# Kernel optimization log

Measured on AMD Instinct MI355X. Metric: run time of the kernel, lower is better.

Reference implementation:

```python
import jax, jax.numpy as jnp
import numpy as np

NF = 64      # feature channels
DG = 8       # deformable groups
KH = 3       # kernel size
K = KH * KH  # kernel points
B, H, W = 2, 256, 256


def conv2d(x, w, b):
    # 3x3, stride 1, pad 1, NCHW
    y = jax.lax.conv_general_dilated(x, w, (1, 1), [(1, 1), (1, 1)],
                                     dimension_numbers=('NCHW', 'OIHW', 'NCHW'))
    return y + b[None, :, None, None]


def bilinear_gather(img, py, px):
    # img: [B,G,Cg,H,W]; py,px: [B,G,Kd,H,W] float pixel coords (zero padding outside)
    # returns [B,G,Cg,Kd,H,W]
    b, g, cg, h, w = img.shape
    kd = py.shape[2]
    y0 = jnp.floor(py)
    x0 = jnp.floor(px)
    wy = py - y0
    wx = px - x0
    imgf = img.reshape(b, g, cg, h * w)

    def tap(yi, xi, wt):
        valid = (yi >= 0) & (yi <= h - 1) & (xi >= 0) & (xi <= w - 1)
        idx = (jnp.clip(yi, 0, h - 1) * w + jnp.clip(xi, 0, w - 1)).astype(jnp.int32)
        idxf = idx.reshape(b, g, 1, kd * h * w)
        v = jnp.take_along_axis(imgf, jnp.broadcast_to(idxf, (b, g, cg, kd * h * w)), axis=-1)
        v = v.reshape(b, g, cg, kd, h, w)
        return v * (wt * valid)[:, :, None]

    return (tap(y0, x0, (1 - wy) * (1 - wx)) + tap(y0, x0 + 1, (1 - wy) * wx)
            + tap(y0 + 1, x0, wy * (1 - wx)) + tap(y0 + 1, x0 + 1, wy * wx))


def setup_inputs() -> dict:
    key = jax.random.key(0)
    ks = jax.random.split(key, 8)
    s = 0.05
    return {
        'nbr': jax.random.normal(ks[0], (B, NF, H, W), jnp.float32),
        'ref': jax.random.normal(ks[1], (B, NF, H, W), jnp.float32),
        'optical_flow': jax.random.normal(ks[2], (B, 2, H, W), jnp.float32),
        'conv1_w': jax.random.normal(ks[3], (NF, 2 * NF, KH, KH), jnp.float32) * s,
        'conv1_b': jnp.zeros((NF,), jnp.float32),
        'om_w': jax.random.normal(ks[4], (DG * 3 * K, NF + 2, KH, KH), jnp.float32) * s,
        'om_b': jnp.zeros((DG * 3 * K,), jnp.float32),
        'dcn_w': jax.random.normal(ks[5], (NF, NF, KH, KH), jnp.float32) * s,
        'dcn_b': jnp.zeros((NF,), jnp.float32),
    }


def reference(nbr, ref, optical_flow, conv1_w, conv1_b, om_w, om_b, dcn_w, dcn_b):
    b, c, h, w = nbr.shape
    dt = nbr.dtype
    gy, gx = jnp.meshgrid(jnp.arange(h, dtype=dt), jnp.arange(w, dtype=dt), indexing='ij')

    # ---- backwarp(nbr, flow): bilinear sample at (x+fx, y+fy), zero padding ----
    py = (gy[None] + optical_flow[:, 1])[:, None, None]  # [B,1,1,H,W]
    px = (gx[None] + optical_flow[:, 0])[:, None, None]
    nbr_warp = bilinear_gather(nbr[:, None], py, px).reshape(b, c, h, w)

    # ---- offset feature ----
    fea = jax.nn.relu(conv2d(jnp.concatenate([nbr_warp, ref], 1), conv1_w, conv1_b))

    # ---- FlowGuidedDCN offset/mask generation ----
    out = conv2d(jnp.concatenate([fea, optical_flow], 1), om_w, om_b)
    o1, o2, mask = jnp.split(out, 3, axis=1)
    offset = jnp.concatenate([o1, o2], 1)                       # [B, 2*DG*K, H, W]
    flow_rep = jnp.tile(optical_flow[:, ::-1], (1, offset.shape[1] // 2, 1, 1))
    offset = offset + flow_rep
    mask = jax.nn.sigmoid(mask)                                 # [B, DG*K, H, W]

    # ---- deformable conv v2 (stride 1, pad 1, dil 1) ----
    off = offset.reshape(b, DG, K, 2, h, w)
    dy, dx = off[:, :, :, 0], off[:, :, :, 1]                   # [B,DG,K,H,W]
    ky, kx = jnp.meshgrid(jnp.arange(KH, dtype=dt), jnp.arange(KH, dtype=dt), indexing='ij')
    base_y = gy[None] - 1 + ky.reshape(-1)[:, None, None]       # [K,H,W]
    base_x = gx[None] - 1 + kx.reshape(-1)[:, None, None]
    spy = base_y[None, None] + dy
    spx = base_x[None, None] + dx

    cg = c // DG
    sampled = bilinear_gather(nbr.reshape(b, DG, cg, h, w), spy, spx)  # [B,DG,Cg,K,H,W]
    m = mask.reshape(b, DG, 1, K, h, w)
    wr = dcn_w.reshape(dcn_w.shape[0], DG, cg, K)
    y = jnp.einsum('bgckhw,ogck->bohw', sampled * m, wr) + dcn_b[None, :, None, None]
    return y
```

## Files before the change

kernel.cpp:

```cpp
#include <hip/hip_runtime.h>
#include <math.h>

#define HW 65536
#define WD 256
#define HT 256

typedef short short8 __attribute__((ext_vector_type(8)));
typedef short sh4 __attribute__((ext_vector_type(4)));
typedef float f32x4 __attribute__((ext_vector_type(4)));
typedef __bf16 bf16x8 __attribute__((ext_vector_type(8)));
typedef __bf16 bf16x4 __attribute__((ext_vector_type(4)));

__device__ __forceinline__ short f2bf(float f) {
    union { float f; unsigned u; } v; v.f = f;
    unsigned r = (v.u + 0x7fffu + ((v.u >> 16) & 1u)) >> 16;
    return (short)r;
}

__device__ __forceinline__ float bf2f(short s) {
    union { unsigned u; float f; } v;
    v.u = ((unsigned)(unsigned short)s) << 16;
    return v.f;
}

__device__ __forceinline__ int iclamp(int v, int lo, int hi) {
    return v < lo ? lo : (v > hi ? hi : v);
}

struct Taps {
    int i00, i01, i10, i11;
    float w00, w01, w10, w11;
};

__device__ __forceinline__ Taps make_taps(float py, float px) {
    float fy0 = floorf(py), fx0 = floorf(px);
    float wy = py - fy0, wx = px - fx0;
    int y0 = (int)fy0, x0 = (int)fx0;
    int y1 = y0 + 1, x1 = x0 + 1;
    float vy0 = (y0 >= 0 && y0 <= HT - 1) ? 1.f : 0.f;
    float vy1 = (y1 >= 0 && y1 <= HT - 1) ? 1.f : 0.f;
    float vx0 = (x0 >= 0 && x0 <= WD - 1) ? 1.f : 0.f;
    float vx1 = (x1 >= 0 && x1 <= WD - 1) ? 1.f : 0.f;
    int yc0 = iclamp(y0, 0, HT - 1), yc1 = iclamp(y1, 0, HT - 1);
    int xc0 = iclamp(x0, 0, WD - 1), xc1 = iclamp(x1, 0, WD - 1);
    Taps t;
    t.i00 = yc0 * WD + xc0; t.i01 = yc0 * WD + xc1;
    t.i10 = yc1 * WD + xc0; t.i11 = yc1 * WD + xc1;
    t.w00 = (1.f - wy) * (1.f - wx) * vy0 * vx0;
    t.w01 = (1.f - wy) * wx * vy0 * vx1;
    t.w10 = wy * (1.f - wx) * vy1 * vx0;
    t.w11 = wy * wx * vy1 * vx1;
    return t;
}

__global__ __launch_bounds__(256) void pack_nbr_kernel(
    const float* __restrict__ nbr, short* __restrict__ N2)
{
    __shared__ short tile[64 * 66];
    int blk = blockIdx.x;
    int b = blk >> 10;
    int grp = blk & 1023;
    int px = threadIdx.x & 63;
    int qq = threadIdx.x >> 6;
    int pos = grp * 64 + px;

    const float* nb = nbr + (size_t)b * 64 * HW;
    #pragma unroll
    for (int j = 0; j < 16; ++j) {
        int c = qq * 16 + j;
        tile[px * 66 + c] = f2bf(nb[c * HW + pos]);
    }
    __syncthreads();

    short* xo = N2 + (size_t)b * HW * 64;
    #pragma unroll
    for (int f8 = threadIdx.x; f8 < 512; f8 += 256) {
        int g = f8 >> 6;
        int p = f8 & 63;
        short8 v;
        #pragma unroll
        for (int j = 0; j < 8; ++j) v[j] = tile[p * 66 + g * 8 + j];
        *(short8*)(xo + ((size_t)g * HW + grp * 64 + p) * 8) = v;
    }
}

__global__ __launch_bounds__(256) void pack_x1_kernel(
    const short* __restrict__ N2, const float* __restrict__ ref,
    const float* __restrict__ flow, short* __restrict__ X1)
{
    __shared__ short tile[64 * 136];
    int blk = blockIdx.x;
    int b = blk >> 10;
    int grp = blk & 1023;
    int px = threadIdx.x & 63;
    int qq = threadIdx.x >> 6;
    int pos = grp * 64 + px;
    int yy = pos >> 8, xx = pos & 255;

    float fx = flow[b * 2 * HW + pos];
    float fy = flow[b * 2 * HW + HW + pos];
    Taps tp = make_taps((float)yy + fy, (float)xx + fx);

    const short* n2b = N2 + (size_t)b * HW * 64;
    const float* rf = ref + (size_t)b * 64 * HW;

    #pragma unroll
    for (int gi = 0; gi < 2; ++gi) {
        int g = qq * 2 + gi;
        const short* nbg = n2b + (size_t)g * HW * 8;
        short8 a00 = *(const short8*)(nbg + (size_t)tp.i00 * 8);
        short8 a01 = *(const short8*)(nbg + (size_t)tp.i01 * 8);
        short8 a10 = *(const short8*)(nbg + (size_t)tp.i10 * 8);
        short8 a11 = *(const short8*)(nbg + (size_t)tp.i11 * 8);
        union { bf16x8 bv; short8 s; } u;
        #pragma unroll
        for (int c = 0; c < 8; ++c) {
            float s = tp.w00 * bf2f(a00[c]) + tp.w01 * bf2f(a01[c]) +
                      tp.w10 * bf2f(a10[c]) + tp.w11 * bf2f(a11[c]);
            u.bv[c] = (__bf16)s;
        }
        *(short8*)(&tile[px * 136 + g * 8]) = u.s;
    }
    #pragma unroll
    for (int j = 0; j < 16; ++j) {
        int c = qq * 16 + j;
        tile[px * 136 + 64 + c] = f2bf(rf[c * HW + pos]);
    }
    __syncthreads();

    short* xo = X1 + ((size_t)b * HW + grp * 64) * 128;
    #pragma unroll
    for (int f8 = threadIdx.x; f8 < 1024; f8 += 256) {
        int p = (f8 * 8) >> 7;
        int c = (f8 * 8) & 127;
        short8 v;
        #pragma unroll
        for (int j = 0; j < 8; ++j) v[j] = tile[p * 136 + c + j];
        *(short8*)(xo + f8 * 8) = v;
    }
}

__global__ __launch_bounds__(256) void repack_w1_kernel(
    const float* __restrict__ w, short* __restrict__ wr)
{
    int t = blockIdx.x * 256 + threadIdx.x;
    int j = t & 7, q = (t >> 3) & 3, l = (t >> 5) & 15;
    int nt = (t >> 9) & 3, kc = t >> 11;
    int k = kc * 32 + q * 8 + j;
    int rs = k >> 7, c = k & 127;
    int n = nt * 16 + l;
    wr[t] = f2bf(w[(n * 128 + c) * 9 + rs]);
}

__global__ __launch_bounds__(256) void repack_w2_kernel(
    const float* __restrict__ w, short* __restrict__ wr)
{
    int t = blockIdx.x * 256 + threadIdx.x;
    if (t >= 155648) return;
    int j = t & 7, q = (t >> 3) & 3, l = (t >> 5) & 15;
    int nt = (t >> 9) & 15, kc = t >> 13;
    int n = nt * 16 + l;
    float v = 0.f;
    if (kc < 18) {
        int k = kc * 32 + q * 8 + j;
        int rs = k >> 6, c = k & 63;
        if (n < 216) v = w[(n * 66 + c) * 9 + rs];
    } else {
        int k18 = q * 8 + j;
        if (k18 < 18 && n < 216) {
            int tap = k18 >> 1, u = k18 & 1;
            v = w[(n * 66 + 64 + u) * 9 + tap];
        }
    }
    wr[t] = f2bf(v);
}

__global__ __launch_bounds__(256) void repack_dcn_kernel(
    const float* __restrict__ w, short* __restrict__ wr)
{
    int t = blockIdx.x * 256 + threadIdx.x;
    int j = t & 7, q = (t >> 3) & 3, l = (t >> 5) & 15;
    int rem = t >> 9;
    int nt = rem & 3;
    int gkc = rem >> 2;
    int kc = gkc % 3, g = gkc / 3;
    int Kidx = kc * 32 + q * 8 + j;
    int k = Kidx >> 3, c = Kidx & 7;
    int och = nt * 16 + l;
    float v = (k < 9) ? w[(och * 64 + g * 8 + c) * 9 + k] : 0.f;
    wr[t] = f2bf(v);
}

#define PADC1 128
__global__ __launch_bounds__(256) void conv1_mfma_kernel(
    const short* __restrict__ X1, const float* __restrict__ bias,
    const short* __restrict__ wr, short* __restrict__ X2)
{
    __shared__ short lds[198 * PADC1];
    const int tid = threadIdx.x;
    const int w = __builtin_amdgcn_readfirstlane(tid >> 6);
    const int l15 = tid & 15;
    const int q = (tid >> 4) & 3;
    const int blk = ((blockIdx.x & 7) << 8) | (blockIdx.x >> 3);
    const int xseg = blk & 3;
    const int yy = (blk >> 2) & 255;
    const int b = blk >> 10;
    const int x0 = xseg * 64;

    const short* xin = X1 + (size_t)b * HW * 128;
    for (int i = tid; i < 198 * 16; i += 256) {
        int c16 = i & 15;
        int pix = i >> 4;
        int r = pix / 66, xx = pix % 66;
        int gy = yy + r - 1, gx = x0 + xx - 1;
        short8 v = {0, 0, 0, 0, 0, 0, 0, 0};
        if (gy >= 0 && gy < HT && gx >= 0 && gx < WD)
            v = *(const short8*)(xin + ((size_t)((gy << 8) + gx)) * 128 + c16 * 8);
        *(short8*)(&lds[pix * PADC1 + (c16 ^ (pix & 7)) * 8]) = v;
    }
    __syncthreads();

    f32x4 acc[4] = {{0,0,0,0},{0,0,0,0},{0,0,0,0},{0,0,0,0}};
    const int bbase = l15 * 4 + q;

    #define LOADB1(kc_) (*(const short8*)(wr + ((size_t)(((kc_) * 4 + w) * 64 + bbase)) * 8))
    #define COMP1(kc_, bf_) { \
        int rs_ = (kc_) >> 2, cc_ = (kc_) & 3; \
        int r_ = rs_ / 3, s_ = rs_ % 3; \
        int rowb_ = r_ * 66 + s_ + l15; \
        _Pragma("unroll") \
        for (int mt = 0; mt < 4; ++mt) { \
            int row_ = rowb_ + mt * 16; \
            int col16_ = (cc_ * 4 + q) ^ (row_ & 7); \
            short8 a_ = *(const short8*)(&lds[row_ * PADC1 + col16_ * 8]); \
            acc[mt] = __builtin_amdgcn_mfma_f32_16x16x32_bf16(a_, bf_, acc[mt], 0, 0, 0); \
        } }

    short8 bA = LOADB1(0), bB;
    #pragma unroll 1
    for (int jj = 0; jj < 18; ++jj) {
        int kc0 = 2 * jj;
        bB = LOADB1(kc0 + 1);
        COMP1(kc0, bA);
        int kc2 = kc0 + 2; if (kc2 > 35) kc2 = 35;
        bA = LOADB1(kc2);
        COMP1(kc0 + 1, bB);
    }
    #undef LOADB1
    #undef COMP1

    float bv = bias[w * 16 + l15];
    short* xo = X2 + (size_t)b * HW * 64;
    #pragma unroll
    for (int mt = 0; mt < 4; ++mt) {
        #pragma unroll
        for (int rg = 0; rg < 4; ++rg) {
            int px = x0 + mt * 16 + q * 4 + rg;
            float v = fmaxf(acc[mt][rg] + bv, 0.f);
            xo[((size_t)((yy << 8) + px)) * 64 + w * 16 + l15] = f2bf(v);
        }
    }
}

#define PADX2 64
__global__ __launch_bounds__(256, 2) void om_mfma_kernel(
    const short* __restrict__ X2, const float* __restrict__ flow,
    const short* __restrict__ wr, const float* __restrict__ bias,
    float* __restrict__ OFF, short* __restrict__ MB)
{
    __shared__ __align__(16) char ldsraw[67584];
    short* ldsA = (short*)ldsraw;
    short* A18  = (short*)(ldsraw + 49920);
    float* ldsT = (float*)ldsraw;

    const int tid = threadIdx.x;
    const int w = __builtin_amdgcn_readfirstlane(tid >> 6);
    const int l15 = tid & 15;
    const int q = (tid >> 4) & 3;
    const int blk = ((blockIdx.x & 7) << 7) | (blockIdx.x >> 3);
    const int xseg = blk & 1;
    const int yy = (blk >> 1) & 255;
    const int b = blk >> 9;
    const int x0 = xseg * 128;

    const short* xin = X2 + (size_t)b * HW * 64;
    #pragma unroll
    for (int r = 0; r < 3; ++r) {
        int gy = yy + r - 1;
        for (int i = tid; i < 130 * 8; i += 256) {
            int xx = i >> 3, c8 = i & 7;
            int gx = x0 + xx - 1;
            short8 v = {0, 0, 0, 0, 0, 0, 0, 0};
            if (gy >= 0 && gy < HT && gx >= 0 && gx < WD)
                v = *(const short8*)(xin + ((size_t)((gy << 8) + gx)) * 64 + c8 * 8);
            int pix = r * 130 + xx;
            *(short8*)(&ldsA[pix * PADX2 + (c8 ^ (pix & 7)) * 8]) = v;
        }
    }
    for (int i = tid; i < 128 * 32; i += 256) {
        int p = i >> 5, kk = i & 31;
        short v = 0;
        if (kk < 18) {
            int tap = kk >> 1, u = kk & 1;
            int gy = yy + tap / 3 - 1, gx = x0 + p + tap % 3 - 1;
            if (gy >= 0 && gy < HT && gx >= 0 && gx < WD)
                v = f2bf(flow[(size_t)(b * 2 + u) * HW + (gy << 8) + gx]);
        }
        A18[p * 34 + kk] = v;
    }
    __syncthreads();

    f32x4 acc[4][8];
    #pragma unroll
    for (int i = 0; i < 4; ++i)
        #pragma unroll
        for (int mt = 0; mt < 8; ++mt) acc[i][mt] = (f32x4){0, 0, 0, 0};

    const int bbase = l15 * 4 + q;

    #define LOADB2(dst_, kc_) { \
        _Pragma("unroll") \
        for (int i = 0; i < 4; ++i) \
            dst_[i] = *(const short8*)(wr + ((size_t)(((kc_) * 16 + w * 4 + i) * 64 + bbase)) * 8); }
    #define COMP2(kc_, bf_) { \
        int rs_ = (kc_) >> 1, half_ = (kc_) & 1; \
        int r_ = rs_ / 3, s_ = rs_ % 3; \
        int rowb_ = r_ * 130 + s_ + l15; \
        _Pragma("unroll") \
        for (int mt = 0; mt < 8; ++mt) { \
            int row_ = rowb_ + mt * 16; \
            int col16_ = (half_ * 4 + q) ^ (row_ & 7); \
            short8 a_ = *(const short8*)(&ldsA[row_ * PADX2 + col16_ * 8]); \
            _Pragma("unroll") \
            for (int i = 0; i < 4; ++i) \
                acc[i][mt] = __builtin_amdgcn_mfma_f32_16x16x32_bf16(a_, bf_[i], acc[i][mt], 0, 0, 0); \
        } }

    short8 bA[4], bB[4];
    LOADB2(bA, 0);
    #pragma unroll 1
    for (int jj = 0; jj < 9; ++jj) {
        int kc0 = 2 * jj;
        LOADB2(bB, kc0 + 1);
        COMP2(kc0, bA);
        LOADB2(bA, kc0 + 2);
        COMP2(kc0 + 1, bB);
    }
    #pragma unroll
    for (int mt = 0; mt < 8; ++mt) {
        short8 a_ = *(const short8*)(&A18[(mt * 16 + l15) * 34 + q * 8]);
        #pragma unroll
        for (int i = 0; i < 4; ++i)
            acc[i][mt] = __builtin_amdgcn_mfma_f32_16x16x32_bf16(a_, bA[i], acc[i][mt], 0, 0, 0);
    }
    #undef LOADB2
    #undef COMP2

    #pragma unroll 1
    for (int pass = 0; pass < 2; ++pass) {
        __syncthreads();
        if ((w >> 1) == pass) {
            int ochl_base = (w & 1) * 64;
            #pragma unroll
            for (int i = 0; i < 4; ++i) {
                int ochl = ochl_base + i * 16 + l15;
                #pragma unroll
                for (int mt = 0; mt < 8; ++mt)
                    #pragma unroll
                    for (int rg = 0; rg < 4; ++rg)
                        ldsT[ochl * 132 + mt * 16 + q * 4 + rg] = acc[i][mt][rg];
            }
        }
        __syncthreads();
        for (int f = tid; f < 128 * 32; f += 256) {
            int chl = f >> 5, p16 = (f & 31) * 4;
            int ch = pass * 128 + chl;
            if (ch < 216) {
                f32x4 v = *(const f32x4*)(&ldsT[chl * 132 + p16]);
                float bv = bias[ch];
                if (ch < 144) {
                    v[0] += bv; v[1] += bv; v[2] += bv; v[3] += bv;
                    *(f32x4*)(&OFF[((size_t)b * 144 + ch) * HW + (yy << 8) + x0 + p16]) = v;
                } else {
                    union { bf16x4 bv4; sh4 s4; } u;
                    #pragma unroll
                    for (int j = 0; j < 4; ++j) {
                        float m = 1.f / (1.f + __expf(-(v[j] + bv)));
                        u.bv4[j] = (__bf16)m;
                    }
                    *(sh4*)(&MB[((size_t)b * 72 + (ch - 144)) * HW + (yy << 8) + x0 + p16]) = u.s4;
                }
            }
        }
    }
}

__global__ __launch_bounds__(256) void dcn_mfma_kernel(
    const float* __restrict__ OFF,
    const short* __restrict__ MB,
    const float* __restrict__ flow,
    const short* __restrict__ N2,
    const short* __restrict__ wrd,
    const float* __restrict__ bias,
    float* __restrict__ out)
{
    __shared__ __align__(16) char ldsraw[26624];
    short* bufA = (short*)ldsraw;
    short* bufB = (short*)(ldsraw + 13312);
    float* ldsT = (float*)ldsraw;

    const int tid = threadIdx.x;
    const int w = __builtin_amdgcn_readfirstlane(tid >> 6);
    const int l15 = tid & 15;
    const int q = (tid >> 4) & 3;
    const int qq = tid >> 6;
    const int px = tid & 63;

    const int blk = ((blockIdx.x & 7) << 8) | (blockIdx.x >> 3);
    const int b = blk >> 10;
    const int grp = blk & 1023;
    const int pos0 = grp * 64;
    const int pos = pos0 + px;
    const int yy = pos >> 8, xx = pos & 255;

    const float* offb = OFF + (size_t)b * 144 * HW + pos;
    const short* mbp  = MB + (size_t)b * 72 * HW + pos;
    const float fx = flow[b * 2 * HW + pos];
    const float fy = flow[b * 2 * HW + HW + pos];
    const short* n2b = N2 + (size_t)b * HW * 64;

    {
        short8 z = {0, 0, 0, 0, 0, 0, 0, 0};
        #pragma unroll
        for (int it = 0; it < 3; ++it) {
            int k = qq + 4 * it;
            if (k >= 9) {
                *(short8*)(&bufA[px * 104 + k * 8]) = z;
                *(short8*)(&bufB[px * 104 + k * 8]) = z;
            }
        }
    }

    f32x4 acc[4] = {{0,0,0,0},{0,0,0,0},{0,0,0,0},{0,0,0,0}};

    float rdy[3], rdx[3];
    short rms[3];
    #pragma unroll
    for (int it = 0; it < 3; ++it) {
        int k = qq + 4 * it;
        rdy[it] = 0.f; rdx[it] = 0.f; rms[it] = 0;
        if (k < 9) {
            rdy[it] = offb[(size_t)(2 * k) * HW];
            rdx[it] = offb[(size_t)(2 * k + 1) * HW];
            rms[it] = mbp[(size_t)k * HW];
        }
    }

    {
        const short* nbg = n2b;
        float w00[3], w01[3], w10[3], w11[3];
        short8 a00[3], a01[3], a10[3], a11[3];
        #pragma unroll
        for (int it = 0; it < 3; ++it) {
            int k = qq + 4 * it;
            if (k < 9) {
                float dy = rdy[it] + fy, dx = rdx[it] + fx;
                float m = bf2f(rms[it]);
                Taps tp = make_taps((float)(yy - 1 + k / 3) + dy,
                                    (float)(xx - 1 + k % 3) + dx);
                w00[it] = tp.w00 * m; w01[it] = tp.w01 * m;
                w10[it] = tp.w10 * m; w11[it] = tp.w11 * m;
                a00[it] = *(const short8*)(nbg + (size_t)tp.i00 * 8);
                a01[it] = *(const short8*)(nbg + (size_t)tp.i01 * 8);
                a10[it] = *(const short8*)(nbg + (size_t)tp.i10 * 8);
                a11[it] = *(const short8*)(nbg + (size_t)tp.i11 * 8);
            }
        }
        #pragma unroll
        for (int it = 0; it < 3; ++it) {
            int k = qq + 4 * it;
            if (k < 9) {
                rdy[it] = offb[(size_t)(18 + 2 * k) * HW];
                rdx[it] = offb[(size_t)(18 + 2 * k + 1) * HW];
                rms[it] = mbp[(size_t)(9 + k) * HW];
            }
        }
        #pragma unroll
        for (int it = 0; it < 3; ++it) {
            int k = qq + 4 * it;
            if (k < 9) {
                union { bf16x8 bv; short8 s; } u;
                #pragma unroll
                for (int c = 0; c < 8; ++c) {
                    float s = w00[it] * bf2f(a00[it][c]) + w01[it] * bf2f(a01[it][c]) +
                              w10[it] * bf2f(a10[it][c]) + w11[it] * bf2f(a11[it][c]);
                    u.bv[c] = (__bf16)s;
                }
                *(short8*)(&bufA[px * 104 + k * 8]) = u.s;
            }
        }
    }
    __syncthreads();

    #pragma unroll 1
    for (int g = 0; g < 8; ++g) {
        short* cur = (g & 1) ? bufB : bufA;
        short* nxt = (g & 1) ? bufA : bufB;

        float w00[3], w01[3], w10[3], w11[3];
        short8 a00[3], a01[3], a10[3], a11[3];
        if (g < 7) {
            const short* nbg = n2b + (size_t)(g + 1) * HW * 8;
            #pragma unroll
            for (int it = 0; it < 3; ++it) {
                int k = qq + 4 * it;
                if (k < 9) {
                    float dy = rdy[it] + fy, dx = rdx[it] + fx;
                    float m = bf2f(rms[it]);
                    Taps tp = make_taps((float)(yy - 1 + k / 3) + dy,
                                        (float)(xx - 1 + k % 3) + dx);
                    w00[it] = tp.w00 * m; w01[it] = tp.w01 * m;
                    w10[it] = tp.w10 * m; w11[it] = tp.w11 * m;
                    a00[it] = *(const short8*)(nbg + (size_t)tp.i00 * 8);
                    a01[it] = *(const short8*)(nbg + (size_t)tp.i01 * 8);
                    a10[it] = *(const short8*)(nbg + (size_t)tp.i10 * 8);
                    a11[it] = *(const short8*)(nbg + (size_t)tp.i11 * 8);
                }
            }
            if (g < 6) {
                #pragma unroll
                for (int it = 0; it < 3; ++it) {
                    int k = qq + 4 * it;
                    if (k < 9) {
                        rdy[it] = offb[(size_t)((g + 2) * 18 + 2 * k) * HW];
                        rdx[it] = offb[(size_t)((g + 2) * 18 + 2 * k + 1) * HW];
                        rms[it] = mbp[(size_t)((g + 2) * 9 + k) * HW];
                    }
                }
            }
        }

        #pragma unroll
        for (int kc = 0; kc < 3; ++kc) {
            short8 bfrag = *(const short8*)(wrd +
                ((size_t)(((g * 3 + kc) * 4 + w) * 64 + l15 * 4 + q)) * 8);
            #pragma unroll
            for (int mt = 0; mt < 4; ++mt) {
                short8 a = *(const short8*)(&cur[(mt * 16 + l15) * 104 + kc * 32 + q * 8]);
                acc[mt] = __builtin_amdgcn_mfma_f32_16x16x32_bf16(a, bfrag, acc[mt], 0, 0, 0);
            }
        }

        if (g < 7) {
            #pragma unroll
            for (int it = 0; it < 3; ++it) {
                int k = qq + 4 * it;
                if (k < 9) {
                    union { bf16x8 bv; short8 s; } u;
                    #pragma unroll
                    for (int c = 0; c < 8; ++c) {
                        float s = w00[it] * bf2f(a00[it][c]) + w01[it] * bf2f(a01[it][c]) +
                                  w10[it] * bf2f(a10[it][c]) + w11[it] * bf2f(a11[it][c]);
                        u.bv[c] = (__bf16)s;
                    }
                    *(short8*)(&nxt[px * 104 + k * 8]) = u.s;
                }
            }
        }
        __syncthreads();
    }

    #pragma unroll
    for (int mt = 0; mt < 4; ++mt)
        *(f32x4*)(&ldsT[(w * 16 + l15) * 68 + mt * 16 + q * 4]) = acc[mt];
    __syncthreads();
    float* ob = out + (size_t)b * 64 * HW + pos0;
    #pragma unroll
    for (int f = tid; f < 1024; f += 256) {
        int och = f >> 4, p4 = (f & 15) * 4;
        f32x4 v = *(const f32x4*)(&ldsT[och * 68 + p4]);
        float bv = bias[och];
        v[0] += bv; v[1] += bv; v[2] += bv; v[3] += bv;
        *(f32x4*)(&ob[(size_t)och * HW + p4]) = v;
    }
}

extern "C" void kernel_launch(void* const* d_in, const int* in_sizes, int n_in,
                              void* d_out, int out_size, void* d_ws, size_t ws_size,
                              hipStream_t stream)
{
    const float* nbr  = (const float*)d_in[0];
    const float* ref  = (const float*)d_in[1];
    const float* flow = (const float*)d_in[2];
    const float* c1w  = (const float*)d_in[3];
    const float* c1b  = (const float*)d_in[4];
    const float* omw  = (const float*)d_in[5];
    const float* omb  = (const float*)d_in[6];
    const float* dw   = (const float*)d_in[7];
    const float* db   = (const float*)d_in[8];
    float* out = (float*)d_out;

    char* wsb = (char*)d_ws;
    short* X1    = (short*)(wsb);
    short* X2    = (short*)(wsb + 33554432);
    short* N2    = (short*)(wsb + 50331648);
    float* OFF   = (float*)(wsb + 67108864);
    short* MB    = (short*)(wsb + 142606336);
    short* wr1   = (short*)(wsb + 161480704);
    short* wr2   = (short*)(wsb + 161628160);
    short* wrd   = (short*)(wsb + 161939456);

    repack_w1_kernel<<<288, 256, 0, stream>>>(c1w, wr1);
    repack_w2_kernel<<<608, 256, 0, stream>>>(omw, wr2);
    repack_dcn_kernel<<<192, 256, 0, stream>>>(dw, wrd);
    pack_nbr_kernel<<<2048, 256, 0, stream>>>(nbr, N2);
    pack_x1_kernel<<<2048, 256, 0, stream>>>(N2, ref, flow, X1);
    conv1_mfma_kernel<<<2048, 256, 0, stream>>>(X1, c1b, wr1, X2);
    om_mfma_kernel<<<1024, 256, 0, stream>>>(X2, flow, wr2, omb, OFF, MB);
    dcn_mfma_kernel<<<2048, 256, 0, stream>>>(OFF, MB, flow, N2, wrd, db, out);
}
```

Measured before the change: 325.4 us.

## Retile conv1 so each block computes four rows with all output channels per wave

The conv1 MFMA kernel now has each block cover four output rows by 64 pixels instead of one row, with each wave owning one row and all 64 output channels. Input channels are staged through shared memory in two halves of 64. This cuts redundant halo loads across blocks (6 input rows for 4 outputs instead of 3 for 1) and reuses each A fragment across four B tiles. The grid shrinks from 2048 to 512 blocks, and the 64 accumulators per lane raise register pressure, which may reduce occupancy.

```diff
diff --git a/kernel.cpp b/kernel.cpp
--- a/kernel.cpp
+++ b/kernel.cpp
@@ -191,73 +191,93 @@
     wr[t] = f2bf(v);
 }
 
-#define PADC1 128
 __global__ __launch_bounds__(256) void conv1_mfma_kernel(
     const short* __restrict__ X1, const float* __restrict__ bias,
     const short* __restrict__ wr, short* __restrict__ X2)
 {
-    __shared__ short lds[198 * PADC1];
+    __shared__ short lds[396 * 64];
     const int tid = threadIdx.x;
     const int w = __builtin_amdgcn_readfirstlane(tid >> 6);
     const int l15 = tid & 15;
     const int q = (tid >> 4) & 3;
-    const int blk = ((blockIdx.x & 7) << 8) | (blockIdx.x >> 3);
+    const int blk = ((blockIdx.x & 7) << 6) | (blockIdx.x >> 3);
     const int xseg = blk & 3;
-    const int yy = (blk >> 2) & 255;
-    const int b = blk >> 10;
+    const int yq = (blk >> 2) & 63;
+    const int b = blk >> 8;
     const int x0 = xseg * 64;
+    const int y0r = yq * 4;
 
     const short* xin = X1 + (size_t)b * HW * 128;
-    for (int i = tid; i < 198 * 16; i += 256) {
-        int c16 = i & 15;
-        int pix = i >> 4;
-        int r = pix / 66, xx = pix % 66;
-        int gy = yy + r - 1, gx = x0 + xx - 1;
-        short8 v = {0, 0, 0, 0, 0, 0, 0, 0};
-        if (gy >= 0 && gy < HT && gx >= 0 && gx < WD)
-            v = *(const short8*)(xin + ((size_t)((gy << 8) + gx)) * 128 + c16 * 8);
-        *(short8*)(&lds[pix * PADC1 + (c16 ^ (pix & 7)) * 8]) = v;
-    }
-    __syncthreads();
-
-    f32x4 acc[4] = {{0,0,0,0},{0,0,0,0},{0,0,0,0},{0,0,0,0}};
     const int bbase = l15 * 4 + q;
 
-    #define LOADB1(kc_) (*(const short8*)(wr + ((size_t)(((kc_) * 4 + w) * 64 + bbase)) * 8))
-    #define COMP1(kc_, bf_) { \
-        int rs_ = (kc_) >> 2, cc_ = (kc_) & 3; \
+    f32x4 acc[4][4];
+    #pragma unroll
+    for (int ot = 0; ot < 4; ++ot)
+        #pragma unroll
+        for (int mt = 0; mt < 4; ++mt) acc[ot][mt] = (f32x4){0, 0, 0, 0};
+
+    #define LOADB1(dst_, t_) { \
+        int kc_ = ((t_) >> 1) * 4 + h * 2 + ((t_) & 1); \
+        _Pragma("unroll") \
+        for (int ot = 0; ot < 4; ++ot) \
+            dst_[ot] = *(const short8*)(wr + ((size_t)((kc_ * 4 + ot) * 64 + bbase)) * 8); }
+    #define COMP1(t_, bf_) { \
+        int rs_ = (t_) >> 1, cch_ = (t_) & 1; \
         int r_ = rs_ / 3, s_ = rs_ % 3; \
-        int rowb_ = r_ * 66 + s_ + l15; \
+        int prow_ = (w + r_) * 66 + s_ + l15; \
         _Pragma("unroll") \
         for (int mt = 0; mt < 4; ++mt) { \
-            int row_ = rowb_ + mt * 16; \
-            int col16_ = (cc_ * 4 + q) ^ (row_ & 7); \
-            short8 a_ = *(const short8*)(&lds[row_ * PADC1 + col16_ * 8]); \
-            acc[mt] = __builtin_amdgcn_mfma_f32_16x16x32_bf16(a_, bf_, acc[mt], 0, 0, 0); \
+            int pr_ = prow_ + mt * 16; \
+            int col16_ = (cch_ * 4 + q) ^ (pr_ & 7); \
+            short8 a_ = *(const short8*)(&lds[pr_ * 64 + col16_ * 8]); \
+            _Pragma("unroll") \
+            for (int ot = 0; ot < 4; ++ot) \
+                acc[ot][mt] = __builtin_amdgcn_mfma_f32_16x16x32_bf16(a_, bf_[ot], acc[ot][mt], 0, 0, 0); \
         } }
 
-    short8 bA = LOADB1(0), bB;
     #pragma unroll 1
-    for (int jj = 0; jj < 18; ++jj) {
-        int kc0 = 2 * jj;
-        bB = LOADB1(kc0 + 1);
-        COMP1(kc0, bA);
-        int kc2 = kc0 + 2; if (kc2 > 35) kc2 = 35;
-        bA = LOADB1(kc2);
-        COMP1(kc0 + 1, bB);
+    for (int h = 0; h < 2; ++h) {
+        __syncthreads();
+        for (int i = tid; i < 396 * 8; i += 256) {
+            int c8 = i & 7;
+            int pix = i >> 3;
+            int r = pix / 66, xx = pix - r * 66;
+            int gy = y0r + r - 1, gx = x0 + xx - 1;
+            short8 v = {0, 0, 0, 0, 0, 0, 0, 0};
+            if (gy >= 0 && gy < HT && gx >= 0 && gx < WD)
+                v = *(const short8*)(xin + ((size_t)((gy << 8) + gx)) * 128 + h * 64 + c8 * 8);
+            *(short8*)(&lds[pix * 64 + ((c8 ^ (pix & 7)) * 8)]) = v;
+        }
+        __syncthreads();
+
+        short8 bA[4], bB[4];
+        LOADB1(bA, 0);
+        #pragma unroll 1
+        for (int jj = 0; jj < 9; ++jj) {
+            int t0 = 2 * jj;
+            LOADB1(bB, t0 + 1);
+            COMP1(t0, bA);
+            int t2 = t0 + 2; if (t2 > 17) t2 = 17;
+            LOADB1(bA, t2);
+            COMP1(t0 + 1, bB);
+        }
     }
     #undef LOADB1
     #undef COMP1
 
-    float bv = bias[w * 16 + l15];
     short* xo = X2 + (size_t)b * HW * 64;
-    #pragma unroll
-    for (int mt = 0; mt < 4; ++mt) {
-        #pragma unroll
-        for (int rg = 0; rg < 4; ++rg) {
-            int px = x0 + mt * 16 + q * 4 + rg;
-            float v = fmaxf(acc[mt][rg] + bv, 0.f);
-            xo[((size_t)((yy << 8) + px)) * 64 + w * 16 + l15] = f2bf(v);
+    const int gyy = y0r + w;
+    #pragma unroll
+    for (int ot = 0; ot < 4; ++ot) {
+        float bv = bias[ot * 16 + l15];
+        #pragma unroll
+        for (int mt = 0; mt < 4; ++mt) {
+            #pragma unroll
+            for (int rg = 0; rg < 4; ++rg) {
+                int gpx = x0 + mt * 16 + q * 4 + rg;
+                float v = fmaxf(acc[ot][mt][rg] + bv, 0.f);
+                xo[((size_t)((gyy << 8) + gpx)) * 64 + ot * 16 + l15] = f2bf(v);
+            }
         }
     }
 }
@@ -615,7 +635,7 @@
     repack_dcn_kernel<<<192, 256, 0, stream>>>(dw, wrd);
     pack_nbr_kernel<<<2048, 256, 0, stream>>>(nbr, N2);
     pack_x1_kernel<<<2048, 256, 0, stream>>>(N2, ref, flow, X1);
-    conv1_mfma_kernel<<<2048, 256, 0, stream>>>(X1, c1b, wr1, X2);
+    conv1_mfma_kernel<<<512, 256, 0, stream>>>(X1, c1b, wr1, X2);
     om_mfma_kernel<<<1024, 256, 0, stream>>>(X2, flow, wr2, omb, OFF, MB);
     dcn_mfma_kernel<<<2048, 256, 0, stream>>>(OFF, MB, flow, N2, wrd, db, out);
 }
```

Measured after the change: 321.9 us (median of 2 runs). About the same (-1.1%).
